# Performance work log

Measured on AMD Instinct MI355X. Metric: run time of the kernel, lower is better.

The kernel has to match this reference:

```python
import jax, jax.numpy as jnp
import numpy as np

N_NODES = 100000


def gcn_conv(x, edge_index, W, b, n_nodes):
    # PyG GCNConv: h = x @ W; add self-loops; symmetric normalization; aggregate to dst; + bias
    h = x @ W  # [N, out]
    loop = jnp.arange(n_nodes, dtype=edge_index.dtype)
    src = jnp.concatenate([edge_index[0], loop])
    dst = jnp.concatenate([edge_index[1], loop])
    ones = jnp.ones(src.shape[0], dtype=h.dtype)
    deg = jax.ops.segment_sum(ones, dst, num_segments=n_nodes)  # in-degree incl. self-loop
    dinv = jnp.where(deg > 0, jax.lax.rsqrt(deg), 0.0)
    norm = dinv[src] * dinv[dst]  # [E+N]
    msgs = h[src] * norm[:, None]  # gather + scale
    out = jax.ops.segment_sum(msgs, dst, num_segments=n_nodes)  # scatter-add
    return out + b


def setup_inputs() -> dict:
    key = jax.random.key(0)
    k1, k2, k3, k4 = jax.random.split(key, 4)
    x = jax.random.normal(k1, (N_NODES, 256), dtype=jnp.float32)
    edge_index = jax.random.randint(k2, (2, 3200000), 0, N_NODES, dtype=jnp.int64)
    W1 = jax.random.normal(k3, (256, 64), dtype=jnp.float32) * (1.0 / np.sqrt(256))
    b1 = jnp.zeros((64,), dtype=jnp.float32)
    W2 = jax.random.normal(k4, (64, 40), dtype=jnp.float32) * (1.0 / np.sqrt(64))
    b2 = jnp.zeros((40,), dtype=jnp.float32)
    return {"x": x, "edge_index": edge_index, "W1": W1, "b1": b1, "W2": W2, "b2": b2}


def reference(x, edge_index, W1, b1, W2, b2):
    n = x.shape[0]
    h = gcn_conv(x, edge_index, W1, b1, n)
    h = jax.nn.relu(h)
    h = gcn_conv(h, edge_index, W2, b2, n)
    return jax.nn.log_softmax(h, axis=1)
```

## Files before the change

### kernel.cpp

```cpp
#include <hip/hip_runtime.h>
#include <hip/hip_bf16.h>
#include <math.h>

static constexpr int NN    = 100000;
static constexpr int BSH   = 9;
static constexpr int NBUCK = (NN + 511) >> 9;
static constexpr int EPB   = 8192;
static constexpr int CAP   = 24576;

typedef __attribute__((ext_vector_type(8))) short short8;
typedef __attribute__((ext_vector_type(4))) float f32x4;
typedef __attribute__((ext_vector_type(2))) float f32x2;

#if defined(__has_builtin)
#  if __has_builtin(__builtin_amdgcn_cvt_pk_f32_fp8) && __has_builtin(__builtin_amdgcn_cvt_pk_fp8_f32)
#    define USE_HW_FP8 1
#  endif
#endif
#ifndef USE_HW_FP8
#  define USE_HW_FP8 0
#endif

__device__ __forceinline__ short f2bf(float f) {
    __hip_bfloat16 h = __float2bfloat16(f);
    return __builtin_bit_cast(short, h);
}

__device__ __forceinline__ float fp8_dec_sw(unsigned b) {
    unsigned u = ((b & 0x80u) << 24) | ((b & 0x7Fu) << 20);
    return __builtin_bit_cast(float, u) * 0x1p120f;
}
__device__ __forceinline__ unsigned fp8_enc_sw(float f) {
    unsigned u = __builtin_bit_cast(unsigned, f * 0x1p-120f);
    unsigned s = (u >> 24) & 0x80u;
    unsigned mag = u & 0x7FFFFFFFu;
    unsigned t = mag + 0x7FFFFu + ((mag >> 20) & 1u);
    unsigned r = t >> 20;
    if (r > 0x7Eu) r = 0x7Eu;
    return s | r;
}

template<bool HI>
__device__ __forceinline__ f32x2 dec2w(unsigned u) {
#if USE_HW_FP8
    return __builtin_amdgcn_cvt_pk_f32_fp8(u, HI);
#else
    unsigned w = HI ? (u >> 16) : u;
    f32x2 r;
    r.x = fp8_dec_sw(w & 0xFFu);
    r.y = fp8_dec_sw((w >> 8) & 0xFFu);
    return r;
#endif
}
__device__ __forceinline__ unsigned enc2(float a, float b) {
#if USE_HW_FP8
    return (unsigned)__builtin_amdgcn_cvt_pk_fp8_f32(a, b, 0, false);
#else
    return fp8_enc_sw(a) | (fp8_enc_sw(b) << 8);
#endif
}

__device__ __forceinline__ void acc8(f32x2* a, uint2 u) {
    a[0] += dec2w<false>(u.x);
    a[1] += dec2w<true>(u.x);
    a[2] += dec2w<false>(u.y);
    a[3] += dec2w<true>(u.y);
}
__device__ __forceinline__ void acc8s(f32x2* a, uint2 u, float ds) {
    f32x2 w = {ds, ds};
    a[0] = dec2w<false>(u.x) * w + a[0];
    a[1] = dec2w<true>(u.x)  * w + a[1];
    a[2] = dec2w<false>(u.y) * w + a[2];
    a[3] = dec2w<true>(u.y)  * w + a[3];
}

__device__ __forceinline__ long long ldidx(const void* __restrict__ p, long long i, int is64) {
    if (is64) return ((const long long* __restrict__)p)[i];
    return (long long)((const int* __restrict__)p)[i];
}

template<int K, int NCOLS, int KT, int NT>
__device__ __forceinline__ void packB_dev(const float* __restrict__ W,
                                          short* __restrict__ P, int t) {
    if (t >= KT * NT * 64) return;
    int kt = t / (NT * 64);
    int nt = (t / 64) % NT;
    int l  = t & 63;
    int g  = l >> 4;
#pragma unroll
    for (int e = 0; e < 8; ++e) {
        int k   = kt * 32 + g * 8 + e;
        int col = nt * 16 + (l & 15);
        float v = (col < NCOLS) ? W[k * NCOLS + col] : 0.0f;
        P[t * 8 + e] = f2bf(v);
    }
}

__global__ void __launch_bounds__(256)
k_init(const unsigned int* __restrict__ e32, int* __restrict__ flag,
       int* __restrict__ gcur,
       const float* __restrict__ W1, short* __restrict__ pB1,
       const float* __restrict__ W2, short* __restrict__ pB2) {
    int blk = blockIdx.x, tid = threadIdx.x;
    if (blk == 0) {
        if (tid < NBUCK) gcur[tid] = 0;
        __shared__ int any_nz;
        if (tid == 0) any_nz = 0;
        __syncthreads();
        unsigned int nz = 0;
        for (int w = 1 + 2 * tid; w < 4096; w += 512)
            nz |= e32[w];
        if (nz) atomicOr(&any_nz, 1);
        __syncthreads();
        if (tid == 0) *flag = (any_nz == 0) ? 1 : 0;
    } else if (blk <= 8) {
        packB_dev<256, 64, 8, 4>(W1, pB1, (blk - 1) * 256 + tid);
    } else {
        packB_dev<64, 40, 2, 3>(W2, pB2, (blk - 9) * 256 + tid);
    }
}

__global__ void __launch_bounds__(1024)
k_build_gemm1(const void* __restrict__ eidx, const int* __restrict__ flag, long long E,
              int nsblk, int ngblk, int* __restrict__ gcur, unsigned* __restrict__ ebuf,
              const float* __restrict__ X, const short* __restrict__ pB1,
              unsigned char* __restrict__ H, int n) {
    int bid = (int)blockIdx.x;
    int mn = nsblk < ngblk ? nsblk : ngblk;
    int role, idx;
    if (bid < 2 * mn) { role = bid & 1; idx = bid >> 1; }
    else {
        int rem = bid - 2 * mn;
        role = (nsblk > ngblk) ? 0 : 1;
        idx = mn + rem;
    }
    if (role == 0) {
        __shared__ int h[NBUCK];
        for (int b = threadIdx.x; b < NBUCK; b += 1024) h[b] = 0;
        __syncthreads();
        int is64 = *flag;
        long long base = (long long)idx * EPB;
        long long end  = base + EPB < E ? base + EPB : E;
        unsigned sv[8], dv[8];
        bool ok[8];
#pragma unroll
        for (int k = 0; k < 8; ++k) {
            long long e = base + (long long)k * 1024 + threadIdx.x;
            ok[k] = (e < end);
            if (ok[k]) {
                sv[k] = (unsigned)ldidx(eidx, e, is64);
                dv[k] = (unsigned)ldidx(eidx, E + e, is64);
                atomicAdd(&h[dv[k] >> BSH], 1);
            }
        }
        __syncthreads();
        for (int b = threadIdx.x; b < NBUCK; b += 1024)
            h[b] = atomicAdd(&gcur[b], h[b]);
        __syncthreads();
#pragma unroll
        for (int k = 0; k < 8; ++k) {
            if (ok[k]) {
                int bk = dv[k] >> BSH;
                int pos = atomicAdd(&h[bk], 1);
                ebuf[(long long)bk * CAP + pos] = sv[k] | ((dv[k] & 511u) << 17);
            }
        }
    } else {
        __shared__ alignas(16) short sW[8 * 4 * 512];
        short8* dst = (short8*)sW;
        const short8* src = (const short8*)pB1;
        int tid = threadIdx.x;
        for (int i = tid; i < 2048; i += 1024) dst[i] = src[i];
        __syncthreads();

        int wave = tid >> 6, lane = tid & 63;
        int g = lane >> 4;
        int arow = idx * 256 + wave * 16 + (lane & 15);

        f32x4 acc[4];
#pragma unroll
        for (int nt = 0; nt < 4; ++nt) acc[nt] = (f32x4){0.f, 0.f, 0.f, 0.f};

#pragma unroll
        for (int kt = 0; kt < 8; ++kt) {
            short8 a;
            if (arow < n) {
                const float* xr = X + (long long)arow * 256;
                int k0 = kt * 32 + g * 8;
                float4 u = *(const float4*)(xr + k0);
                float4 v = *(const float4*)(xr + k0 + 4);
                a[0] = f2bf(u.x); a[1] = f2bf(u.y); a[2] = f2bf(u.z); a[3] = f2bf(u.w);
                a[4] = f2bf(v.x); a[5] = f2bf(v.y); a[6] = f2bf(v.z); a[7] = f2bf(v.w);
            } else {
                a = (short8){0, 0, 0, 0, 0, 0, 0, 0};
            }
#pragma unroll
            for (int nt = 0; nt < 4; ++nt) {
                short8 bfr = dst[(kt * 4 + nt) * 64 + lane];
                acc[nt] = __builtin_amdgcn_mfma_f32_16x16x32_bf16(a, bfr, acc[nt], 0, 0, 0);
            }
        }

        int c = lane & 15;
        int orow_base = idx * 256 + wave * 16 + g * 4;
#pragma unroll
        for (int r = 0; r < 4; ++r) {
            int orow = orow_base + r;
            if (orow < n) {
                unsigned char* hp = H + (long long)orow * 64;
#pragma unroll
                for (int p = 0; p < 4; p += 2) {
                    unsigned wrd = enc2(acc[p][r], acc[p + 1][r]);
                    hp[p * 16 + c]        = (unsigned char)(wrd & 0xFFu);
                    hp[(p + 1) * 16 + c]  = (unsigned char)((wrd >> 8) & 0xFFu);
                }
            }
        }
    }
}

__global__ void __launch_bounds__(1024)
k_bucket_csr(const unsigned* __restrict__ ebuf, const int* __restrict__ gcnt,
             int* __restrict__ rowst, float* __restrict__ dinv,
             int* __restrict__ csr, int n) {
    __shared__ int cnt[512];
    __shared__ int cursor[512];
    __shared__ int woff[8];
    __shared__ int bs_sh;
    int b = blockIdx.x;
    int t = threadIdx.x;
    int cb = gcnt[b];
    long long rbase = (long long)b * CAP;
    if (t == 0) bs_sh = 0;
    if (t < 512) cnt[t] = 0;
    __syncthreads();
    if (t < b) atomicAdd(&bs_sh, gcnt[t]);
    for (int i = t; i < cb; i += 1024) {
        unsigned ed = ebuf[rbase + i];
        atomicAdd(&cnt[ed >> 17], 1);
    }
    __syncthreads();
    int bs = bs_sh;
    if (b == NBUCK - 1 && t == 0) rowst[n] = bs + cb;
    int v = 0, ps = 0;
    if (t < 512) {
        v = cnt[t];
        ps = v;
        int lane = t & 63;
#pragma unroll
        for (int off = 1; off < 64; off <<= 1) {
            int up = __shfl_up(ps, off);
            if (lane >= off) ps += up;
        }
        if (lane == 63) woff[t >> 6] = ps;
    }
    __syncthreads();
    if (t == 0) {
        int run = 0;
#pragma unroll
        for (int i = 0; i < 8; ++i) { int x = woff[i]; woff[i] = run; run += x; }
    }
    __syncthreads();
    if (t < 512) {
        int incl  = ps + woff[t >> 6];
        int start = bs + incl - v;
        int gnode = (b << BSH) + t;
        if (gnode < n) {
            rowst[gnode] = start;
            dinv[gnode]  = rsqrtf((float)(v + 1));
        }
        cursor[t] = start;
    }
    __syncthreads();
    for (int i = t; i < cb; i += 1024) {
        unsigned ed = ebuf[rbase + i];
        int pos = atomicAdd(&cursor[ed >> 17], 1);
        csr[pos] = (int)(ed & 0x1FFFFu);
    }
}

template<int K, int NCOLS, int KT, int NT, bool ABF16>
__global__ void __launch_bounds__(256)
k_mfma_gemm(const void* __restrict__ Xv, const short* __restrict__ packedB,
            const float* __restrict__ dinv, unsigned char* __restrict__ H, int n) {
    __shared__ alignas(16) short sW[KT * NT * 512];
    short8* dst = (short8*)sW;
    const short8* src = (const short8*)packedB;
    constexpr int TOT8 = KT * NT * 64;
    for (int i = threadIdx.x; i < TOT8; i += 256) dst[i] = src[i];
    __syncthreads();

    int wave = threadIdx.x >> 6, lane = threadIdx.x & 63;
    int g = lane >> 4;
    int arow = blockIdx.x * 64 + wave * 16 + (lane & 15);

    f32x4 acc[NT];
#pragma unroll
    for (int nt = 0; nt < NT; ++nt) acc[nt] = (f32x4){0.f, 0.f, 0.f, 0.f};

#pragma unroll
    for (int kt = 0; kt < KT; ++kt) {
        short8 a;
        if (arow < n) {
            int k0 = kt * 32 + g * 8;
            if (ABF16) {
                const short* xr = (const short*)Xv + (long long)arow * K;
                a = *(const short8*)(xr + k0);
            } else {
                const float* xr = (const float*)Xv + (long long)arow * K;
                float4 u = *(const float4*)(xr + k0);
                float4 v = *(const float4*)(xr + k0 + 4);
                a[0] = f2bf(u.x); a[1] = f2bf(u.y); a[2] = f2bf(u.z); a[3] = f2bf(u.w);
                a[4] = f2bf(v.x); a[5] = f2bf(v.y); a[6] = f2bf(v.z); a[7] = f2bf(v.w);
            }
        } else {
            a = (short8){0, 0, 0, 0, 0, 0, 0, 0};
        }
#pragma unroll
        for (int nt = 0; nt < NT; ++nt) {
            short8 bfr = dst[(kt * NT + nt) * 64 + lane];
            acc[nt] = __builtin_amdgcn_mfma_f32_16x16x32_bf16(a, bfr, acc[nt], 0, 0, 0);
        }
    }

    int c = lane & 15;
    int orow_base = blockIdx.x * 64 + wave * 16 + g * 4;
#pragma unroll
    for (int r = 0; r < 4; ++r) {
        int orow = orow_base + r;
        if (orow < n) {
            float di = dinv[orow];
            float v[NT];
#pragma unroll
            for (int nt = 0; nt < NT; ++nt) v[nt] = acc[nt][r] * di;
            unsigned char* hp = H + (long long)orow * NCOLS;
#pragma unroll
            for (int p = 0; p < NT; p += 2) {
                unsigned wrd = enc2(v[p], (p + 1 < NT) ? v[p + 1] : 0.0f);
                int col0 = p * 16 + c;
                if (col0 < NCOLS) hp[col0] = (unsigned char)(wrd & 0xFFu);
                if (p + 1 < NT) {
                    int col1 = col0 + 16;
                    if (col1 < NCOLS) hp[col1] = (unsigned char)((wrd >> 8) & 0xFFu);
                }
            }
        }
    }
}

__global__ void __launch_bounds__(256)
k_gather_relu(const int* __restrict__ rowst, const int* __restrict__ csr,
              const unsigned char* __restrict__ h1s, const float* __restrict__ dinv,
              const float* __restrict__ b, unsigned short* __restrict__ out, int n) {
    long long gid = (long long)blockIdx.x * blockDim.x + threadIdx.x;
    int node = (int)(gid >> 3);
    int fe   = (int)(gid & 7);
    if (node >= n) return;
    int jb = rowst[node], je = rowst[node + 1];
    unsigned feoff = (unsigned)fe << 3;

    f32x2 a0[4], a1[4], a2[4], a3[4];
#pragma unroll
    for (int q = 0; q < 4; ++q) {
        a0[q] = (f32x2){0.f, 0.f}; a1[q] = (f32x2){0.f, 0.f};
        a2[q] = (f32x2){0.f, 0.f}; a3[q] = (f32x2){0.f, 0.f};
    }

    int j = jb;
    for (; j + 3 < je; j += 4) {
        int s0 = csr[j], s1 = csr[j + 1], s2 = csr[j + 2], s3 = csr[j + 3];
        float ds0 = dinv[s0], ds1 = dinv[s1], ds2 = dinv[s2], ds3 = dinv[s3];
        uint2 u0 = *(const uint2*)(h1s + (((unsigned)s0 << 6) + feoff));
        uint2 u1 = *(const uint2*)(h1s + (((unsigned)s1 << 6) + feoff));
        uint2 u2 = *(const uint2*)(h1s + (((unsigned)s2 << 6) + feoff));
        uint2 u3 = *(const uint2*)(h1s + (((unsigned)s3 << 6) + feoff));
        acc8s(a0, u0, ds0);
        acc8s(a1, u1, ds1);
        acc8s(a2, u2, ds2);
        acc8s(a3, u3, ds3);
    }
    for (; j < je; ++j) {
        int s0 = csr[j];
        float ds0 = dinv[s0];
        uint2 u0 = *(const uint2*)(h1s + (((unsigned)s0 << 6) + feoff));
        acc8s(a0, u0, ds0);
    }
#pragma unroll
    for (int q = 0; q < 4; ++q) a0[q] += (a1[q] + a2[q]) + a3[q];

    float dn = dinv[node];
    uint2 self = *(const uint2*)(h1s + (((unsigned)node << 6) + feoff));
    acc8s(a0, self, dn);
    unsigned short r[8];
#pragma unroll
    for (int q = 0; q < 4; ++q) {
        float v0 = fmaxf(a0[q].x * dn + b[8 * fe + 2 * q],     0.0f);
        float v1 = fmaxf(a0[q].y * dn + b[8 * fe + 2 * q + 1], 0.0f);
        r[2 * q]     = (unsigned short)f2bf(v0);
        r[2 * q + 1] = (unsigned short)f2bf(v1);
    }
    uint4 pk;
    pk.x = (unsigned)r[0] | ((unsigned)r[1] << 16);
    pk.y = (unsigned)r[2] | ((unsigned)r[3] << 16);
    pk.z = (unsigned)r[4] | ((unsigned)r[5] << 16);
    pk.w = (unsigned)r[6] | ((unsigned)r[7] << 16);
    ((uint4*)(out + (long long)node * 64))[fe] = pk;
}

__global__ void __launch_bounds__(256)
k_gather_lsm(const int* __restrict__ rowst, const int* __restrict__ csr,
             const unsigned char* __restrict__ h2s, const float* __restrict__ dinv,
             const float* __restrict__ b, float* __restrict__ out, int n) {
    long long gid = (long long)blockIdx.x * blockDim.x + threadIdx.x;
    int node = (int)(gid >> 3);
    int fe   = (int)(gid & 7);
    if (node >= n) return;
    bool act = (fe < 5);
    int jb = rowst[node], je = rowst[node + 1];
    unsigned feoff = (unsigned)fe << 3;

    f32x2 a0[4], a1[4], a2[4], a3[4];
#pragma unroll
    for (int q = 0; q < 4; ++q) {
        a0[q] = (f32x2){0.f, 0.f}; a1[q] = (f32x2){0.f, 0.f};
        a2[q] = (f32x2){0.f, 0.f}; a3[q] = (f32x2){0.f, 0.f};
    }

    int j = jb;
    for (; j + 3 < je; j += 4) {
        int s0 = csr[j], s1 = csr[j + 1], s2 = csr[j + 2], s3 = csr[j + 3];
        if (act) {
            uint2 u0 = *(const uint2*)(h2s + ((unsigned)s0 * 40u + feoff));
            uint2 u1 = *(const uint2*)(h2s + ((unsigned)s1 * 40u + feoff));
            uint2 u2 = *(const uint2*)(h2s + ((unsigned)s2 * 40u + feoff));
            uint2 u3 = *(const uint2*)(h2s + ((unsigned)s3 * 40u + feoff));
            acc8(a0, u0);
            acc8(a1, u1);
            acc8(a2, u2);
            acc8(a3, u3);
        }
    }
    for (; j < je; ++j) {
        int s0 = csr[j];
        if (act) {
            uint2 u0 = *(const uint2*)(h2s + ((unsigned)s0 * 40u + feoff));
            acc8(a0, u0);
        }
    }
#pragma unroll
    for (int q = 0; q < 4; ++q) a0[q] += (a1[q] + a2[q]) + a3[q];

    float va[8];
    float mloc = -INFINITY;
    if (act) {
        uint2 self = *(const uint2*)(h2s + ((unsigned)node * 40u + feoff));
        acc8(a0, self);
        float di = dinv[node];
#pragma unroll
        for (int q = 0; q < 4; ++q) {
            va[2 * q]     = a0[q].x * di + b[8 * fe + 2 * q];
            va[2 * q + 1] = a0[q].y * di + b[8 * fe + 2 * q + 1];
            mloc = fmaxf(mloc, fmaxf(va[2 * q], va[2 * q + 1]));
        }
    }
    float m = mloc;
    m = fmaxf(m, __shfl_xor(m, 1));
    m = fmaxf(m, __shfl_xor(m, 2));
    m = fmaxf(m, __shfl_xor(m, 4));
    float ex = 0.0f;
    if (act) {
#pragma unroll
        for (int k = 0; k < 8; ++k) ex += __expf(va[k] - m);
    }
    ex += __shfl_xor(ex, 1);
    ex += __shfl_xor(ex, 2);
    ex += __shfl_xor(ex, 4);
    float lse = __logf(ex);
    if (act) {
        float4 r0 = make_float4(va[0] - m - lse, va[1] - m - lse,
                                va[2] - m - lse, va[3] - m - lse);
        float4 r1 = make_float4(va[4] - m - lse, va[5] - m - lse,
                                va[6] - m - lse, va[7] - m - lse);
        *(float4*)(out + (long long)node * 40 + 8 * fe)     = r0;
        *(float4*)(out + (long long)node * 40 + 8 * fe + 4) = r1;
    }
}

extern "C" void kernel_launch(void* const* d_in, const int* in_sizes, int n_in,
                              void* d_out, int out_size, void* d_ws, size_t ws_size,
                              hipStream_t stream) {
    const float* x  = (const float*)d_in[0];
    const void*  ei = d_in[1];
    const float* W1 = (const float*)d_in[2];
    const float* b1 = (const float*)d_in[3];
    const float* W2 = (const float*)d_in[4];
    const float* b2 = (const float*)d_in[5];
    float* out = (float*)d_out;

    const long long E = (long long)in_sizes[1] / 2;
    const int nsblk = (int)((E + EPB - 1) / EPB);
    const int ngblk = (NN + 255) / 256;

    char* w = (char*)d_ws;
    auto alloc = [&](size_t bytes) -> void* {
        void* p = (void*)w;
        w += (bytes + 255) & ~(size_t)255;
        return p;
    };
    int*      flag    = (int*)     alloc(4);
    int*      gcur    = (int*)     alloc((size_t)NBUCK * 4);
    int*      rowst   = (int*)     alloc(((size_t)NN + 1) * 4);
    float*    dinv    = (float*)   alloc((size_t)NN * 4);
    short*    pB1     = (short*)   alloc((size_t)8 * 4 * 64 * 8 * 2);
    short*    pB2     = (short*)   alloc((size_t)2 * 3 * 64 * 8 * 2);
    int*      csr     = (int*)     alloc((size_t)E * 4);
    unsigned* ebuf    = (unsigned*)alloc((size_t)NBUCK * CAP * 4);
    unsigned char* h1s = (unsigned char*)alloc((size_t)NN * 64);
    unsigned short* agg1 = (unsigned short*)alloc((size_t)NN * 64 * 2);
    unsigned char* h2s = h1s;

    const int B = 256;
    auto cdiv = [](long long a, long long b) { return (int)((a + b - 1) / b); };

    k_init<<<11, B, 0, stream>>>((const unsigned int*)ei, flag, gcur, W1, pB1, W2, pB2);

    k_build_gemm1<<<nsblk + ngblk, 1024, 0, stream>>>(ei, flag, E, nsblk, ngblk,
                                                      gcur, ebuf, x, pB1, h1s, NN);

    k_bucket_csr<<<NBUCK, 1024, 0, stream>>>(ebuf, gcur, rowst, dinv, csr, NN);

    k_gather_relu<<<cdiv((long long)NN * 8, B), B, 0, stream>>>(rowst, csr, h1s, dinv, b1, agg1, NN);

    k_mfma_gemm<64, 40, 2, 3, true><<<cdiv(NN, 64), B, 0, stream>>>(agg1, pB2, dinv, h2s, NN);

    k_gather_lsm<<<cdiv((long long)NN * 8, B), B, 0, stream>>>(rowst, csr, h2s, dinv, b2, out, NN);
}
```

Measured before the change: 180.0 us.

## Stage X rows through LDS with coalesced loads before MFMA in layer-1 GEMM

```diff
diff --git a/kernel.cpp b/kernel.cpp
--- a/kernel.cpp
+++ b/kernel.cpp
@@ -167,54 +167,69 @@
         }
     } else {
         __shared__ alignas(16) short sW[8 * 4 * 512];
+        __shared__ alignas(16) short sX[64 * 264];
         short8* dst = (short8*)sW;
         const short8* src = (const short8*)pB1;
         int tid = threadIdx.x;
         for (int i = tid; i < 2048; i += 1024) dst[i] = src[i];
-        __syncthreads();
 
         int wave = tid >> 6, lane = tid & 63;
         int g = lane >> 4;
-        int arow = idx * 256 + wave * 16 + (lane & 15);
-
-        f32x4 acc[4];
-#pragma unroll
-        for (int nt = 0; nt < 4; ++nt) acc[nt] = (f32x4){0.f, 0.f, 0.f, 0.f};
-
-#pragma unroll
-        for (int kt = 0; kt < 8; ++kt) {
-            short8 a;
-            if (arow < n) {
-                const float* xr = X + (long long)arow * 256;
-                int k0 = kt * 32 + g * 8;
-                float4 u = *(const float4*)(xr + k0);
-                float4 v = *(const float4*)(xr + k0 + 4);
-                a[0] = f2bf(u.x); a[1] = f2bf(u.y); a[2] = f2bf(u.z); a[3] = f2bf(u.w);
-                a[4] = f2bf(v.x); a[5] = f2bf(v.y); a[6] = f2bf(v.z); a[7] = f2bf(v.w);
+        int wig = wave & 3;
+        int grp = wave >> 2;
+
+        int lr = tid >> 4;
+        int c0 = (tid & 15) * 16;
+
+        for (int s = 0; s < 4; ++s) {
+            int grow = idx * 256 + s * 64 + lr;
+            short* xd = &sX[lr * 264 + c0];
+            if (grow < n) {
+                const float* xr = X + (long long)grow * 256 + c0;
+                float4 u0 = *(const float4*)(xr);
+                float4 u1 = *(const float4*)(xr + 4);
+                float4 u2 = *(const float4*)(xr + 8);
+                float4 u3 = *(const float4*)(xr + 12);
+                xd[0]  = f2bf(u0.x); xd[1]  = f2bf(u0.y); xd[2]  = f2bf(u0.z); xd[3]  = f2bf(u0.w);
+                xd[4]  = f2bf(u1.x); xd[5]  = f2bf(u1.y); xd[6]  = f2bf(u1.z); xd[7]  = f2bf(u1.w);
+                xd[8]  = f2bf(u2.x); xd[9]  = f2bf(u2.y); xd[10] = f2bf(u2.z); xd[11] = f2bf(u2.w);
+                xd[12] = f2bf(u3.x); xd[13] = f2bf(u3.y); xd[14] = f2bf(u3.z); xd[15] = f2bf(u3.w);
             } else {
-                a = (short8){0, 0, 0, 0, 0, 0, 0, 0};
+#pragma unroll
+                for (int i = 0; i < 16; ++i) xd[i] = 0;
             }
-#pragma unroll
-            for (int nt = 0; nt < 4; ++nt) {
-                short8 bfr = dst[(kt * 4 + nt) * 64 + lane];
-                acc[nt] = __builtin_amdgcn_mfma_f32_16x16x32_bf16(a, bfr, acc[nt], 0, 0, 0);
-            }
-        }
-
-        int c = lane & 15;
-        int orow_base = idx * 256 + wave * 16 + g * 4;
-#pragma unroll
-        for (int r = 0; r < 4; ++r) {
-            int orow = orow_base + r;
-            if (orow < n) {
-                unsigned char* hp = H + (long long)orow * 64;
-#pragma unroll
-                for (int p = 0; p < 4; p += 2) {
-                    unsigned wrd = enc2(acc[p][r], acc[p + 1][r]);
-                    hp[p * 16 + c]        = (unsigned char)(wrd & 0xFFu);
-                    hp[(p + 1) * 16 + c]  = (unsigned char)((wrd >> 8) & 0xFFu);
+            __syncthreads();
+            if (grp == s) {
+                f32x4 acc[4];
+#pragma unroll
+                for (int nt = 0; nt < 4; ++nt) acc[nt] = (f32x4){0.f, 0.f, 0.f, 0.f};
+                const short* arow_p = &sX[(wig * 16 + (lane & 15)) * 264];
+#pragma unroll
+                for (int kt = 0; kt < 8; ++kt) {
+                    short8 a = *(const short8*)(arow_p + kt * 32 + g * 8);
+#pragma unroll
+                    for (int nt = 0; nt < 4; ++nt) {
+                        short8 bfr = dst[(kt * 4 + nt) * 64 + lane];
+                        acc[nt] = __builtin_amdgcn_mfma_f32_16x16x32_bf16(a, bfr, acc[nt], 0, 0, 0);
+                    }
+                }
+                int c = lane & 15;
+                int orow_base = idx * 256 + s * 64 + wig * 16 + g * 4;
+#pragma unroll
+                for (int r = 0; r < 4; ++r) {
+                    int orow = orow_base + r;
+                    if (orow < n) {
+                        unsigned char* hp = H + (long long)orow * 64;
+#pragma unroll
+                        for (int p = 0; p < 4; p += 2) {
+                            unsigned wrd = enc2(acc[p][r], acc[p + 1][r]);
+                            hp[p * 16 + c]       = (unsigned char)(wrd & 0xFFu);
+                            hp[(p + 1) * 16 + c] = (unsigned char)((wrd >> 8) & 0xFFu);
+                        }
+                    }
                 }
             }
+            __syncthreads();
         }
     }
 }
```

Result: no change. 179.6 us (-0.3%).
